# Kernel tuning notes

Hardware: AMD Instinct MI355X
Metric: run time of the kernel (lower is better)

Reference implementation:

```python
import jax, jax.numpy as jnp
import numpy as np

B, L = 1024, 1024
NCAT, NNUM = 20, 10
CAT_BUCKETS, SEQ_VOCAB = 100000, 50000
E, A, H, QH = 32, 128, 256, 256
TOPK = 30


def _init(key, shape, scale=0.02):
    return scale * jax.random.normal(key, shape, dtype=jnp.float32)


def setup_inputs() -> dict:
    key = jax.random.key(0)
    ks = jax.random.split(key, 24)
    z = lambda *s: jnp.zeros(s, dtype=jnp.float32)
    return {
        "cats": jax.random.randint(ks[0], (B, NCAT), 0, CAT_BUCKETS + 1),
        "nums": jax.random.normal(ks[1], (B, NNUM), dtype=jnp.float32),
        "seqs": jax.random.randint(ks[2], (B, L), 0, SEQ_VOCAB + 1),
        "tgt_ids": jax.random.randint(ks[3], (B,), 0, CAT_BUCKETS + 1),
        "cat_emb": _init(ks[4], (CAT_BUCKETS + 1, E)),
        "seq_emb": _init(ks[5], (SEQ_VOCAB + 1, E)),
        "Wnum": _init(ks[6], (NNUM, E)), "bnum": z(E),
        "Wq": _init(ks[7], (E, A)), "Wk": _init(ks[8], (E, A)), "Wv": _init(ks[9], (E, A)),
        "Wo": _init(ks[10], (A, E)), "bo": z(E),
        "Wpool": _init(ks[11], (NCAT * E, E)), "bpool": z(E),
        "Wmlp": _init(ks[12], (4 * E, H)), "bmlp": z(H),
        "q1_W1": _init(ks[13], (H, QH)), "q1_b1": z(QH),
        "q1_W2": _init(ks[14], (H, QH)), "q1_b2": z(QH),
        "q1_Wp": _init(ks[15], (QH, H)), "q1_bp": z(H),
        "q2_W1": _init(ks[16], (H, QH)), "q2_b1": z(QH),
        "q2_W2": _init(ks[17], (H, QH)), "q2_b2": z(QH),
        "q2_Wp": _init(ks[18], (QH, H)), "q2_bp": z(H),
        "Wout": _init(ks[19], (H, 1)), "bout": z(1),
    }


def _qnn(x, W1, b1, W2, b2, Wp, bp):
    # Quadratic neural block (QIN-style): Hadamard product of two linear maps,
    # projected back with a residual connection. Dropout is identity in eval.
    quad = (x @ W1 + b1) * (x @ W2 + b2)
    return x + quad @ Wp + bp


def reference(cats, nums, seqs, tgt_ids, cat_emb, seq_emb, Wnum, bnum, Wq, Wk, Wv,
              Wo, bo, Wpool, bpool, Wmlp, bmlp,
              q1_W1, q1_b1, q1_W2, q1_b2, q1_Wp, q1_bp,
              q2_W1, q2_b1, q2_W2, q2_b2, q2_Wp, q2_bp, Wout, bout):
    cat_e = cat_emb[cats]                                   # [B, NCAT, E]
    cat_pool = cat_e.reshape(cat_e.shape[0], -1) @ Wpool + bpool   # [B, E]
    num_e = nums @ Wnum + bnum                              # [B, E]
    tgt_e = cat_emb[tgt_ids]                                # [B, E] (tgt_emb shares cat_emb)
    seq_e = seq_emb[seqs]                                   # [B, L, E]

    q = tgt_e @ Wq                                          # [B, A]
    k = seq_e @ Wk                                          # [B, L, A]
    v = seq_e @ Wv                                          # [B, L, A]
    scores = jnp.einsum('ba,bla->bl', q, k) / jnp.sqrt(jnp.float32(A))

    # top-k + scatter mask + masked softmax == softmax over the top-k scores,
    # scattered implicitly via gather of the selected values.
    vals, idx = jax.lax.top_k(scores, TOPK)                 # [B, TOPK]
    w = jax.nn.softmax(vals, axis=1)                        # [B, TOPK]
    v_sel = jnp.take_along_axis(v, idx[:, :, None], axis=1)  # [B, TOPK, A]
    interest = jnp.einsum('bk,bka->ba', w, v_sel) @ Wo + bo  # [B, E]

    fused = jnp.concatenate([tgt_e, interest, cat_pool, num_e], axis=1)  # [B, 4E]
    h = jax.nn.relu(fused @ Wmlp + bmlp)                    # [B, H], dropout=eval
    h = _qnn(h, q1_W1, q1_b1, q1_W2, q1_b2, q1_Wp, q1_bp)
    h = _qnn(h, q2_W1, q2_b1, q2_W2, q2_b2, q2_Wp, q2_bp)
    return (h @ Wout + bout)[:, 0]                          # [B]
```

## Files before the change

### kernel.cpp

```cpp
#include <hip/hip_runtime.h>
#include <hip/hip_fp16.h>

#define B_ 1024
#define L_ 1024
#define NCAT_ 20
#define NNUM_ 10
#define E_ 32
#define A_ 128
#define H_ 256
#define TOPK_ 30
#define INV_SQRT_A 0.08838834764831845f

__device__ __forceinline__ void fma4(float4& a, float s, const float4 w) {
    a.x += s * w.x; a.y += s * w.y; a.z += s * w.z; a.w += s * w.w;
}
__device__ __forceinline__ float4 ldh4(const __half* p) {
    float2 rw = *(const float2*)p;
    const __half2* h = (const __half2*)&rw;
    float2 a = __half22float2(h[0]);
    float2 b = __half22float2(h[1]);
    return make_float4(a.x, a.y, b.x, b.y);
}
__device__ __forceinline__ void ldh24(const __half2* p, float4& w1, float4& w2) {
    float4 rw = *(const float4*)p;
    const __half2* h = (const __half2*)&rw;
    float2 f0 = __half22float2(h[0]), f1 = __half22float2(h[1]);
    float2 f2 = __half22float2(h[2]), f3 = __half22float2(h[3]);
    w1 = make_float4(f0.x, f1.x, f2.x, f3.x);
    w2 = make_float4(f0.y, f1.y, f2.y, f3.y);
}
__device__ __forceinline__ unsigned sortable(float f) {
    unsigned u = __float_as_uint(f);
    return (u & 0x80000000u) ? ~u : (u | 0x80000000u);
}
__device__ __forceinline__ float unsortable(unsigned s) {
    unsigned u = (s & 0x80000000u) ? (s ^ 0x80000000u) : ~s;
    return __uint_as_float(u);
}

#define K1_GRID 1356
__global__ __launch_bounds__(256) void fused_prep_kernel(
    const int* __restrict__ cats, const float* __restrict__ nums,
    const int* __restrict__ tgt_ids, const float* __restrict__ cat_emb,
    const float* __restrict__ Wnum, const float* __restrict__ bnum,
    const float* __restrict__ Wq, const float* __restrict__ Wk,
    const float* __restrict__ Wv, const float* __restrict__ Wo,
    const float* __restrict__ Wpool, const float* __restrict__ bpool,
    const float* __restrict__ seq_emb, const float* __restrict__ Wmlp,
    const float* __restrict__ q1W1, const float* __restrict__ q1W2,
    const float* __restrict__ q2W1, const float* __restrict__ q2W2,
    const float* __restrict__ q1Wp, const float* __restrict__ q2Wp,
    float* __restrict__ p_out, float* __restrict__ fused, float* __restrict__ M,
    __half2* __restrict__ seq_h2, __half2* __restrict__ Wmlp_h2,
    __half2* __restrict__ W12_1, __half2* __restrict__ W12_2,
    __half2* __restrict__ Wp1_h2, __half2* __restrict__ Wp2_h2)
{
    const int blk = blockIdx.x;
    const int t = threadIdx.x;

    if (blk < 256) {
        __shared__ float ce[4][NCAT_ * E_];
        __shared__ float tg[4][E_];
        __shared__ float nm[4][NNUM_];
        __shared__ float qs[4][A_];
        __shared__ float part[8][4][E_];
        const int r0 = blk * 4;

        for (int idx = t; idx < 640; idx += 256) {
            const int q = idx >> 3, f4 = idx & 7;
            const int row = q / 20, cat = q % 20;
            const int tok = cats[(r0 + row) * NCAT_ + cat];
            ((float4*)&ce[row][cat * 32])[f4] =
                ((const float4*)(cat_emb + (size_t)tok * 32))[f4];
        }
        if (t < 32) {
            const int row = t >> 3, f4 = t & 7;
            const int tok = tgt_ids[r0 + row];
            ((float4*)&tg[row][0])[f4] =
                ((const float4*)(cat_emb + (size_t)tok * 32))[f4];
        }
        if (t >= 64 && t < 104) {
            const int x = t - 64;
            nm[x / 10][x % 10] = nums[(r0 + x / 10) * NNUM_ + x % 10];
        }
        __syncthreads();

        {
            const int w = t >> 6, lane = t & 63;
            float q0 = 0.f, q1 = 0.f;
#pragma unroll
            for (int e = 0; e < E_; ++e) {
                float te = tg[w][e];
                q0 += te * Wq[e * A_ + lane];
                q1 += te * Wq[e * A_ + lane + 64];
            }
            qs[w][lane] = q0; qs[w][lane + 64] = q1;
        }

        {
            const int iseg = t >> 5;
            const int row = (t >> 3) & 3;
            const int c0 = (t & 7) * 4;
            float4 acc = make_float4(0.f, 0.f, 0.f, 0.f);
            const int i0 = iseg * 80;
            for (int i = i0; i < i0 + 80; ++i) {
                float4 wv = *(const float4*)(Wpool + i * 32 + c0);
                fma4(acc, ce[row][i], wv);
            }
            *(float4*)&part[iseg][row][c0] = acc;
        }
        __syncthreads();

        if (t < 128) {
            const int row = t >> 5, c = t & 31;
            const int b = r0 + row;
            float s = bpool[c];
#pragma unroll
            for (int g = 0; g < 8; ++g) s += part[g][row][c];
            fused[b * 128 + 64 + c] = s;
            fused[b * 128 + c] = tg[row][c];

            float ne = bnum[c];
#pragma unroll
            for (int n = 0; n < NNUM_; ++n) ne += nm[row][n] * Wnum[n * 32 + c];
            fused[b * 128 + 96 + c] = ne;

            float pv = 0.f;
#pragma unroll 8
            for (int a = 0; a < A_; ++a) pv += Wk[c * A_ + a] * qs[row][a];
            p_out[b * 32 + c] = pv;
        }
        return;
    }

    if (blk < 1280) {
        int x = (blk - 256) * 256 + t;
        for (; x < 800016; x += 1024 * 256) {
            float2 v = ((const float2*)seq_emb)[x];
            seq_h2[x] = __float22half2_rn(v);
        }
        return;
    }

    if (blk < 1284) {
        const int o = (blk - 1280) * 256 + t;
        const int j = o >> 5, e = o & 31;
        float sm = 0.f;
#pragma unroll 8
        for (int a = 0; a < A_; ++a) sm += Wv[j * A_ + a] * Wo[a * E_ + e];
        M[o] = sm;
        return;
    }

    if (blk < 1348) {
        int x = (blk - 1284) * 256 + t;
        for (; x < 65536; x += 64 * 256) {
            W12_1[x] = __float22half2_rn(make_float2(q1W1[x], q1W2[x]));
            W12_2[x] = __float22half2_rn(make_float2(q2W1[x], q2W2[x]));
        }
        return;
    }

    {
        int x = (blk - 1348) * 256 + t;
        for (; x < 16384; x += 8 * 256)
            Wmlp_h2[x] = __float22half2_rn(((const float2*)Wmlp)[x]);
        x = (blk - 1348) * 256 + t;
        for (; x < 32768; x += 8 * 256) {
            Wp1_h2[x] = __float22half2_rn(((const float2*)q1Wp)[x]);
            Wp2_h2[x] = __float22half2_rn(((const float2*)q2Wp)[x]);
        }
    }
}

#define RM 2
__global__ __launch_bounds__(512, 4) void score_mlp_kernel(
    const int* __restrict__ seqs, const __half* __restrict__ seq_h,
    const float* __restrict__ seq_emb, const float* __restrict__ p,
    const float* __restrict__ M, const float* __restrict__ bo,
    const float* __restrict__ fused,
    const __half* __restrict__ Wmlp_h, const float* __restrict__ bmlp,
    const __half2* __restrict__ W12_1, const float* __restrict__ b11,
    const float* __restrict__ b12, const __half* __restrict__ Wp1_h,
    const float* __restrict__ b1p,
    const __half2* __restrict__ W12_2, const float* __restrict__ b21,
    const float* __restrict__ b22, const __half* __restrict__ Wp2_h,
    const float* __restrict__ b2p,
    const float* __restrict__ Wout, const float* __restrict__ bout,
    float* __restrict__ out)
{
    const int b0 = blockIdx.x * RM;
    const int tid = threadIdx.x;

    __shared__ float sc[RM][L_];
    __shared__ float ps[RM][E_];
    __shared__ float sw[RM][32];
    __shared__ int   stok[RM][32];
    __shared__ float xs[RM][128];
    __shared__ float hs[RM][H_];
    __shared__ float ts[RM][H_];
    __shared__ float partA[8][RM][H_];
    __shared__ float partB[8][RM][H_];
    __shared__ float red[8];

    if (tid < RM * 32)
        ps[tid >> 5][tid & 31] = p[(b0 + (tid >> 5)) * 32 + (tid & 31)];
    __syncthreads();

    {
        const int row = tid >> 8;
        const int s = tid & 255;
        const int bb = b0 + row;
#pragma unroll
        for (int jj = 0; jj < 2; ++jj) {
            const int l1 = jj * 512 + s;
            const int l2 = l1 + 256;
            const int tok1 = seqs[bb * L_ + l1];
            const int tok2 = seqs[bb * L_ + l2];
            float4 buf[2][4];
            const float4* r1 = (const float4*)(seq_h + (size_t)tok1 * 32);
            const float4* r2 = (const float4*)(seq_h + (size_t)tok2 * 32);
#pragma unroll
            for (int i = 0; i < 4; ++i) buf[0][i] = r1[i];
#pragma unroll
            for (int i = 0; i < 4; ++i) buf[1][i] = r2[i];

            float acc0 = 0.f, acc1 = 0.f;
#pragma unroll
            for (int i = 0; i < 4; ++i) {
                const __half2* h1 = (const __half2*)&buf[0][i];
                const __half2* h2 = (const __half2*)&buf[1][i];
#pragma unroll
                for (int u = 0; u < 4; ++u) {
                    float2 f1 = __half22float2(h1[u]);
                    float2 f2 = __half22float2(h2[u]);
                    acc0 += f1.x * ps[row][i * 8 + 2 * u] + f1.y * ps[row][i * 8 + 2 * u + 1];
                    acc1 += f2.x * ps[row][i * 8 + 2 * u] + f2.y * ps[row][i * 8 + 2 * u + 1];
                }
            }
            sc[row][l1] = acc0 * INV_SQRT_A;
            sc[row][l2] = acc1 * INV_SQRT_A;
        }
    }
    if (tid < RM * 96) {
        const int r = tid / 96, c0 = tid % 96;
        const int c = (c0 < 32) ? c0 : (c0 + 32);
        xs[r][c] = fused[(b0 + r) * 128 + c];
    }
    __syncthreads();

    if (tid < RM * 64) {
        const int w = tid >> 6;
        const int lane = tid & 63;
        const int bb = b0 + w;

        unsigned long long key[16];
#pragma unroll
        for (int j = 0; j < 16; ++j) {
            const int l = j * 64 + lane;
            key[j] = ((unsigned long long)sortable(sc[w][l]) << 10)
                   | (unsigned)(1023 - l);
        }
#pragma unroll
        for (int a = 0; a < 15; ++a)
#pragma unroll
            for (int j = 0; j < 15 - a; ++j) {
                const bool swp = key[j] < key[j + 1];
                const unsigned long long hi = swp ? key[j + 1] : key[j];
                const unsigned long long lo = swp ? key[j] : key[j + 1];
                key[j] = hi; key[j + 1] = lo;
            }

        float myv = -1e30f; int myl = 0;
        unsigned long long front = key[0];
        for (int k = 0; k < TOPK_; ++k) {
            unsigned long long wk = front;
#pragma unroll
            for (int off = 32; off > 0; off >>= 1) {
                unsigned long long o = __shfl_xor(wk, off);
                if (o > wk) wk = o;
            }
            if (lane == k) {
                myv = unsortable((unsigned)(wk >> 10));
                myl = 1023 - (int)(wk & 1023);
            }
            if (front == wk) {
#pragma unroll
                for (int j = 0; j < 15; ++j) key[j] = key[j + 1];
                key[15] = 0ULL;
                front = key[0];
            }
        }

        float m = myv;
#pragma unroll
        for (int off = 32; off > 0; off >>= 1) m = fmaxf(m, __shfl_xor(m, off));
        float e = (lane < TOPK_) ? expf(myv - m) : 0.f;
        float s = e;
#pragma unroll
        for (int off = 32; off > 0; off >>= 1) s += __shfl_xor(s, off);
        if (lane < TOPK_) {
            sw[w][lane]   = e / s;
            stok[w][lane] = seqs[bb * L_ + myl];
        }

        if (lane < E_) {
            float acc = 0.f;
#pragma unroll
            for (int k = 0; k < TOPK_; ++k)
                acc += sw[w][k] * seq_emb[(size_t)stok[w][k] * 32 + lane];
            sc[w][lane] = acc;
        }
        if (lane < E_) {
            float acc = bo[lane];
#pragma unroll
            for (int j = 0; j < E_; ++j) acc += sc[w][j] * M[j * E_ + lane];
            xs[w][32 + lane] = acc;
        }
    }
    __syncthreads();

    const int cg = tid & 63;
    const int iseg = tid >> 6;
    const int c0 = cg * 4;
    const int rr = tid >> 8;
    const int rc = tid & 255;

    {
        float4 acc[RM];
#pragma unroll
        for (int r = 0; r < RM; ++r) acc[r] = make_float4(0.f, 0.f, 0.f, 0.f);
        const int i0 = iseg * 16;
#pragma unroll
        for (int iq = 0; iq < 4; ++iq) {
            const int i = i0 + iq * 4;
            float4 w[4], xv[RM];
#pragma unroll
            for (int u = 0; u < 4; ++u) w[u] = ldh4(Wmlp_h + (i + u) * H_ + c0);
#pragma unroll
            for (int r = 0; r < RM; ++r) xv[r] = *(const float4*)(&xs[r][i]);
#pragma unroll
            for (int r = 0; r < RM; ++r) {
                fma4(acc[r], xv[r].x, w[0]); fma4(acc[r], xv[r].y, w[1]);
                fma4(acc[r], xv[r].z, w[2]); fma4(acc[r], xv[r].w, w[3]);
            }
        }
#pragma unroll
        for (int r = 0; r < RM; ++r) *(float4*)&partA[iseg][r][c0] = acc[r];
    }
    __syncthreads();
    {
        float s = bmlp[rc];
#pragma unroll
        for (int sg = 0; sg < 8; ++sg) s += partA[sg][rr][rc];
        hs[rr][rc] = fmaxf(s, 0.f);
    }
    __syncthreads();

    const __half2* W12s[2] = { W12_1, W12_2 };
    const float* b1s[2] = { b11, b21 }; const float* b2s[2] = { b12, b22 };
    const __half* Wps[2] = { Wp1_h, Wp2_h }; const float* bps[2] = { b1p, b2p };

    for (int q = 0; q < 2; ++q) {
        const __half2* __restrict__ W12 = W12s[q];
        const __half*  __restrict__ Wp  = Wps[q];
        {
            float4 a1[RM], a2[RM];
#pragma unroll
            for (int r = 0; r < RM; ++r) {
                a1[r] = make_float4(0.f, 0.f, 0.f, 0.f);
                a2[r] = make_float4(0.f, 0.f, 0.f, 0.f);
            }
            const int i0 = iseg * 32;
#pragma unroll 2
            for (int iq = 0; iq < 8; ++iq) {
                const int i = i0 + iq * 4;
                float4 w1[4], w2[4], hv[RM];
#pragma unroll
                for (int u = 0; u < 4; ++u) ldh24(W12 + (i + u) * H_ + c0, w1[u], w2[u]);
#pragma unroll
                for (int r = 0; r < RM; ++r) hv[r] = *(const float4*)(&hs[r][i]);
#pragma unroll
                for (int r = 0; r < RM; ++r) {
                    fma4(a1[r], hv[r].x, w1[0]); fma4(a1[r], hv[r].y, w1[1]);
                    fma4(a1[r], hv[r].z, w1[2]); fma4(a1[r], hv[r].w, w1[3]);
                    fma4(a2[r], hv[r].x, w2[0]); fma4(a2[r], hv[r].y, w2[1]);
                    fma4(a2[r], hv[r].z, w2[2]); fma4(a2[r], hv[r].w, w2[3]);
                }
            }
#pragma unroll
            for (int r = 0; r < RM; ++r) {
                *(float4*)&partA[iseg][r][c0] = a1[r];
                *(float4*)&partB[iseg][r][c0] = a2[r];
            }
        }
        __syncthreads();
        {
            float t1 = b1s[q][rc], t2 = b2s[q][rc];
#pragma unroll
            for (int sg = 0; sg < 8; ++sg) {
                t1 += partA[sg][rr][rc];
                t2 += partB[sg][rr][rc];
            }
            ts[rr][rc] = t1 * t2;
        }
        __syncthreads();

        {
            float4 ap[RM];
#pragma unroll
            for (int r = 0; r < RM; ++r) ap[r] = make_float4(0.f, 0.f, 0.f, 0.f);
            const int i0 = iseg * 32;
#pragma unroll 2
            for (int iq = 0; iq < 8; ++iq) {
                const int i = i0 + iq * 4;
                float4 w[4], tv[RM];
#pragma unroll
                for (int u = 0; u < 4; ++u) w[u] = ldh4(Wp + (i + u) * H_ + c0);
#pragma unroll
                for (int r = 0; r < RM; ++r) tv[r] = *(const float4*)(&ts[r][i]);
#pragma unroll
                for (int r = 0; r < RM; ++r) {
                    fma4(ap[r], tv[r].x, w[0]); fma4(ap[r], tv[r].y, w[1]);
                    fma4(ap[r], tv[r].z, w[2]); fma4(ap[r], tv[r].w, w[3]);
                }
            }
#pragma unroll
            for (int r = 0; r < RM; ++r) *(float4*)&partA[iseg][r][c0] = ap[r];
        }
        __syncthreads();
        {
            float s = bps[q][rc];
#pragma unroll
            for (int sg = 0; sg < 8; ++sg) s += partA[sg][rr][rc];
            hs[rr][rc] += s;
        }
        __syncthreads();
    }

    {
        const int r = (tid >> 7) & (RM - 1);
        const int jj = tid & 127;
        float sum = 0.f;
        if (tid < RM * 128)
            sum = hs[r][jj] * Wout[jj] + hs[r][jj + 128] * Wout[jj + 128];
#pragma unroll
        for (int off = 32; off > 0; off >>= 1) sum += __shfl_down(sum, off);
        if (tid < RM * 128 && (tid & 63) == 0) red[tid >> 6] = sum;
        __syncthreads();
        if (tid < RM) out[b0 + tid] = red[2 * tid] + red[2 * tid + 1] + bout[0];
    }
}

extern "C" void kernel_launch(void* const* d_in, const int* in_sizes, int n_in,
                              void* d_out, int out_size, void* d_ws, size_t ws_size,
                              hipStream_t stream) {
    const int*   cats    = (const int*)d_in[0];
    const float* nums    = (const float*)d_in[1];
    const int*   seqs    = (const int*)d_in[2];
    const int*   tgt_ids = (const int*)d_in[3];
    const float* cat_emb = (const float*)d_in[4];
    const float* seq_emb = (const float*)d_in[5];
    const float* Wnum    = (const float*)d_in[6];
    const float* bnum    = (const float*)d_in[7];
    const float* Wq      = (const float*)d_in[8];
    const float* Wk      = (const float*)d_in[9];
    const float* Wv      = (const float*)d_in[10];
    const float* Wo      = (const float*)d_in[11];
    const float* bo      = (const float*)d_in[12];
    const float* Wpool   = (const float*)d_in[13];
    const float* bpool   = (const float*)d_in[14];
    const float* Wmlp    = (const float*)d_in[15];
    const float* bmlp    = (const float*)d_in[16];
    const float* q1_W1   = (const float*)d_in[17];
    const float* q1_b1   = (const float*)d_in[18];
    const float* q1_W2   = (const float*)d_in[19];
    const float* q1_b2   = (const float*)d_in[20];
    const float* q1_Wp   = (const float*)d_in[21];
    const float* q1_bp   = (const float*)d_in[22];
    const float* q2_W1   = (const float*)d_in[23];
    const float* q2_b1   = (const float*)d_in[24];
    const float* q2_W2   = (const float*)d_in[25];
    const float* q2_b2   = (const float*)d_in[26];
    const float* q2_Wp   = (const float*)d_in[27];
    const float* q2_bp   = (const float*)d_in[28];
    const float* Wout    = (const float*)d_in[29];
    const float* bout    = (const float*)d_in[30];

    float* ws = (float*)d_ws;
    float*   p       = ws;
    float*   fused   = ws + 32768;
    float*   M       = ws + 163840;
    __half2* seq_h2  = (__half2*)(ws + 164864);
    __half2* Wmlp_h2 = (__half2*)(ws + 964928);
    __half2* W12_1   = (__half2*)(ws + 981312);
    __half2* W12_2   = (__half2*)(ws + 1046848);
    __half2* Wp1_h2  = (__half2*)(ws + 1112384);
    __half2* Wp2_h2  = (__half2*)(ws + 1145152);

    float* out = (float*)d_out;

    fused_prep_kernel<<<K1_GRID, 256, 0, stream>>>(
        cats, nums, tgt_ids, cat_emb, Wnum, bnum, Wq, Wk, Wv, Wo,
        Wpool, bpool, seq_emb, Wmlp,
        q1_W1, q1_W2, q2_W1, q2_W2, q1_Wp, q2_Wp,
        p, fused, M, seq_h2, Wmlp_h2, W12_1, W12_2, Wp1_h2, Wp2_h2);

    score_mlp_kernel<<<B_ / RM, 512, 0, stream>>>(
        seqs, (const __half*)seq_h2, seq_emb, p, M, bo, fused,
        (const __half*)Wmlp_h2, bmlp,
        W12_1, q1_b1, q1_b2, (const __half*)Wp1_h2, q1_bp,
        W12_2, q2_b1, q2_b2, (const __half*)Wp2_h2, q2_bp,
        Wout, bout, out);
}
```

Before: 185.4 us.

## Split MLP into separate MFMA kernel with transposed fp16 weights

Moves the MLP and the two quadratic blocks out of the score/top-k kernel into a new kernel that processes 16 rows per block with 16x16x32 fp16 MFMA instructions. The prep kernel now writes transposed fp16 weight copies so MFMA B-operands can be loaded contiguously. The score kernel writes the interest vector to global memory instead of continuing with scalar FMA MLP work. This adds a kernel launch and a global round trip for the fused features, in exchange for much higher MLP throughput and less per-row weight re-reading.

```diff
diff --git a/kernel.cpp b/kernel.cpp
--- a/kernel.cpp
+++ b/kernel.cpp
@@ -11,24 +11,9 @@
 #define TOPK_ 30
 #define INV_SQRT_A 0.08838834764831845f
 
-__device__ __forceinline__ void fma4(float4& a, float s, const float4 w) {
-    a.x += s * w.x; a.y += s * w.y; a.z += s * w.z; a.w += s * w.w;
-}
-__device__ __forceinline__ float4 ldh4(const __half* p) {
-    float2 rw = *(const float2*)p;
-    const __half2* h = (const __half2*)&rw;
-    float2 a = __half22float2(h[0]);
-    float2 b = __half22float2(h[1]);
-    return make_float4(a.x, a.y, b.x, b.y);
-}
-__device__ __forceinline__ void ldh24(const __half2* p, float4& w1, float4& w2) {
-    float4 rw = *(const float4*)p;
-    const __half2* h = (const __half2*)&rw;
-    float2 f0 = __half22float2(h[0]), f1 = __half22float2(h[1]);
-    float2 f2 = __half22float2(h[2]), f3 = __half22float2(h[3]);
-    w1 = make_float4(f0.x, f1.x, f2.x, f3.x);
-    w2 = make_float4(f0.y, f1.y, f2.y, f3.y);
-}
+typedef _Float16 half8 __attribute__((ext_vector_type(8)));
+typedef float f32x4 __attribute__((ext_vector_type(4)));
+
 __device__ __forceinline__ unsigned sortable(float f) {
     unsigned u = __float_as_uint(f);
     return (u & 0x80000000u) ? ~u : (u | 0x80000000u);
@@ -36,6 +21,14 @@
 __device__ __forceinline__ float unsortable(unsigned s) {
     unsigned u = (s & 0x80000000u) ? (s ^ 0x80000000u) : ~s;
     return __uint_as_float(u);
+}
+__device__ __forceinline__ half8 cvt_h8(const float4 u, const float4 v) {
+    half8 a;
+    a[0] = (_Float16)u.x; a[1] = (_Float16)u.y;
+    a[2] = (_Float16)u.z; a[3] = (_Float16)u.w;
+    a[4] = (_Float16)v.x; a[5] = (_Float16)v.y;
+    a[6] = (_Float16)v.z; a[7] = (_Float16)v.w;
+    return a;
 }
 
 #define K1_GRID 1356
@@ -48,12 +41,14 @@
     const float* __restrict__ Wpool, const float* __restrict__ bpool,
     const float* __restrict__ seq_emb, const float* __restrict__ Wmlp,
     const float* __restrict__ q1W1, const float* __restrict__ q1W2,
+    const float* __restrict__ q1Wp,
     const float* __restrict__ q2W1, const float* __restrict__ q2W2,
-    const float* __restrict__ q1Wp, const float* __restrict__ q2Wp,
+    const float* __restrict__ q2Wp,
     float* __restrict__ p_out, float* __restrict__ fused, float* __restrict__ M,
-    __half2* __restrict__ seq_h2, __half2* __restrict__ Wmlp_h2,
-    __half2* __restrict__ W12_1, __half2* __restrict__ W12_2,
-    __half2* __restrict__ Wp1_h2, __half2* __restrict__ Wp2_h2)
+    __half2* __restrict__ seq_h2,
+    __half* __restrict__ WmlpT,
+    __half* __restrict__ W1T1, __half* __restrict__ W2T1, __half* __restrict__ WpT1,
+    __half* __restrict__ W1T2, __half* __restrict__ W2T2, __half* __restrict__ WpT2)
 {
     const int blk = blockIdx.x;
     const int t = threadIdx.x;
@@ -105,7 +100,8 @@
             const int i0 = iseg * 80;
             for (int i = i0; i < i0 + 80; ++i) {
                 float4 wv = *(const float4*)(Wpool + i * 32 + c0);
-                fma4(acc, ce[row][i], wv);
+                acc.x += ce[row][i] * wv.x; acc.y += ce[row][i] * wv.y;
+                acc.z += ce[row][i] * wv.z; acc.w += ce[row][i] * wv.w;
             }
             *(float4*)&part[iseg][row][c0] = acc;
         }
@@ -152,42 +148,47 @@
         return;
     }
 
-    if (blk < 1348) {
-        int x = (blk - 1284) * 256 + t;
-        for (; x < 65536; x += 64 * 256) {
-            W12_1[x] = __float22half2_rn(make_float2(q1W1[x], q1W2[x]));
-            W12_2[x] = __float22half2_rn(make_float2(q2W1[x], q2W2[x]));
-        }
-        return;
-    }
-
     {
-        int x = (blk - 1348) * 256 + t;
-        for (; x < 16384; x += 8 * 256)
-            Wmlp_h2[x] = __float22half2_rn(((const float2*)Wmlp)[x]);
-        x = (blk - 1348) * 256 + t;
-        for (; x < 32768; x += 8 * 256) {
-            Wp1_h2[x] = __float22half2_rn(((const float2*)q1Wp)[x]);
-            Wp2_h2[x] = __float22half2_rn(((const float2*)q2Wp)[x]);
+        int c = (blk - 1284) * 256 + t;
+        for (; c < 53248; c += 72 * 256) {
+            const float* src; __half* dst;
+            int n, k0, K;
+            if (c < 4096) {
+                n = c >> 4; k0 = (c & 15) << 3; K = 128;
+                src = Wmlp; dst = WmlpT;
+            } else {
+                const int c2 = c - 4096;
+                const int m = c2 >> 13, idx = c2 & 8191;
+                n = idx >> 5; k0 = (idx & 31) << 3; K = 256;
+                switch (m) {
+                    case 0: src = q1W1; dst = W1T1; break;
+                    case 1: src = q1W2; dst = W2T1; break;
+                    case 2: src = q1Wp; dst = WpT1; break;
+                    case 3: src = q2W1; dst = W1T2; break;
+                    case 4: src = q2W2; dst = W2T2; break;
+                    default: src = q2Wp; dst = WpT2; break;
+                }
+            }
+            float v[8];
+#pragma unroll
+            for (int i = 0; i < 8; ++i) v[i] = src[(size_t)(k0 + i) * 256 + n];
+            float4 wq;
+            __half2* hp = (__half2*)&wq;
+            hp[0] = __float22half2_rn(make_float2(v[0], v[1]));
+            hp[1] = __float22half2_rn(make_float2(v[2], v[3]));
+            hp[2] = __float22half2_rn(make_float2(v[4], v[5]));
+            hp[3] = __float22half2_rn(make_float2(v[6], v[7]));
+            *(float4*)(dst + (size_t)n * K + k0) = wq;
         }
     }
 }
 
 #define RM 2
-__global__ __launch_bounds__(512, 4) void score_mlp_kernel(
+__global__ __launch_bounds__(512) void score_topk_kernel(
     const int* __restrict__ seqs, const __half* __restrict__ seq_h,
     const float* __restrict__ seq_emb, const float* __restrict__ p,
     const float* __restrict__ M, const float* __restrict__ bo,
-    const float* __restrict__ fused,
-    const __half* __restrict__ Wmlp_h, const float* __restrict__ bmlp,
-    const __half2* __restrict__ W12_1, const float* __restrict__ b11,
-    const float* __restrict__ b12, const __half* __restrict__ Wp1_h,
-    const float* __restrict__ b1p,
-    const __half2* __restrict__ W12_2, const float* __restrict__ b21,
-    const float* __restrict__ b22, const __half* __restrict__ Wp2_h,
-    const float* __restrict__ b2p,
-    const float* __restrict__ Wout, const float* __restrict__ bout,
-    float* __restrict__ out)
+    float* __restrict__ fused)
 {
     const int b0 = blockIdx.x * RM;
     const int tid = threadIdx.x;
@@ -196,12 +197,6 @@
     __shared__ float ps[RM][E_];
     __shared__ float sw[RM][32];
     __shared__ int   stok[RM][32];
-    __shared__ float xs[RM][128];
-    __shared__ float hs[RM][H_];
-    __shared__ float ts[RM][H_];
-    __shared__ float partA[8][RM][H_];
-    __shared__ float partB[8][RM][H_];
-    __shared__ float red[8];
 
     if (tid < RM * 32)
         ps[tid >> 5][tid & 31] = p[(b0 + (tid >> 5)) * 32 + (tid & 31)];
@@ -242,11 +237,6 @@
             sc[row][l2] = acc1 * INV_SQRT_A;
         }
     }
-    if (tid < RM * 96) {
-        const int r = tid / 96, c0 = tid % 96;
-        const int c = (c0 < 32) ? c0 : (c0 + 32);
-        xs[r][c] = fused[(b0 + r) * 128 + c];
-    }
     __syncthreads();
 
     if (tid < RM * 64) {
@@ -315,140 +305,146 @@
             float acc = bo[lane];
 #pragma unroll
             for (int j = 0; j < E_; ++j) acc += sc[w][j] * M[j * E_ + lane];
-            xs[w][32 + lane] = acc;
+            fused[bb * 128 + 32 + lane] = acc;
+        }
+    }
+}
+
+#define GR 16
+#define HSP 260
+#define TSP 264
+__global__ __launch_bounds__(512) void mlp_mfma_kernel(
+    const float* __restrict__ fused,
+    const __half* __restrict__ WmlpT, const float* __restrict__ bmlp,
+    const __half* __restrict__ W1T1, const __half* __restrict__ W2T1,
+    const __half* __restrict__ WpT1,
+    const float* __restrict__ b11, const float* __restrict__ b12,
+    const float* __restrict__ b1p,
+    const __half* __restrict__ W1T2, const __half* __restrict__ W2T2,
+    const __half* __restrict__ WpT2,
+    const float* __restrict__ b21, const float* __restrict__ b22,
+    const float* __restrict__ b2p,
+    const float* __restrict__ Wout, const float* __restrict__ bout,
+    float* __restrict__ out)
+{
+    const int r0 = blockIdx.x * GR;
+    const int tid = threadIdx.x;
+    const int w = tid >> 6;
+    const int l = tid & 63;
+    const int lr = l & 15;
+    const int lk = l >> 4;
+    const int n0 = w * 32;
+
+    __shared__ float hs[GR][HSP];
+    __shared__ __half ts_h[GR][TSP];
+
+    f32x4 hC0, hC1;
+    const f32x4 zf = {0.f, 0.f, 0.f, 0.f};
+
+    {
+        half8 ax[4];
+        const float* xrow = fused + (size_t)(r0 + lr) * 128 + lk * 8;
+#pragma unroll
+        for (int ks = 0; ks < 4; ++ks) {
+            float4 u = *(const float4*)(xrow + ks * 32);
+            float4 v = *(const float4*)(xrow + ks * 32 + 4);
+            ax[ks] = cvt_h8(u, v);
+        }
+#pragma unroll
+        for (int t = 0; t < 2; ++t) {
+            f32x4 c = zf;
+            const __half* wb = WmlpT + (size_t)(n0 + 16 * t + lr) * 128 + lk * 8;
+#pragma unroll
+            for (int ks = 0; ks < 4; ++ks) {
+                half8 b = *(const half8*)(wb + ks * 32);
+                c = __builtin_amdgcn_mfma_f32_16x16x32_f16(ax[ks], b, c, 0, 0, 0);
+            }
+            const int j = n0 + 16 * t + lr;
+            const float bm = bmlp[j];
+#pragma unroll
+            for (int r = 0; r < 4; ++r) {
+                float vv = fmaxf(c[r] + bm, 0.f);
+                if (t == 0) hC0[r] = vv; else hC1[r] = vv;
+                hs[4 * lk + r][j] = vv;
+            }
         }
     }
     __syncthreads();
 
-    const int cg = tid & 63;
-    const int iseg = tid >> 6;
-    const int c0 = cg * 4;
-    const int rr = tid >> 8;
-    const int rc = tid & 255;
+#pragma unroll
+    for (int q = 0; q < 2; ++q) {
+        const __half* W1T = q ? W1T2 : W1T1;
+        const __half* W2T = q ? W2T2 : W2T1;
+        const __half* WpT = q ? WpT2 : WpT1;
+        const float* bb1 = q ? b21 : b11;
+        const float* bb2 = q ? b22 : b12;
+        const float* bbp = q ? b2p : b1p;
+
+        half8 ah[8];
+#pragma unroll
+        for (int ks = 0; ks < 8; ++ks) {
+            const float* hr = &hs[lr][ks * 32 + lk * 8];
+            float4 u = *(const float4*)hr;
+            float4 v = *(const float4*)(hr + 4);
+            ah[ks] = cvt_h8(u, v);
+        }
+#pragma unroll
+        for (int t = 0; t < 2; ++t) {
+            f32x4 t1 = zf, t2 = zf;
+            const __half* w1 = W1T + (size_t)(n0 + 16 * t + lr) * 256 + lk * 8;
+            const __half* w2 = W2T + (size_t)(n0 + 16 * t + lr) * 256 + lk * 8;
+#pragma unroll
+            for (int ks = 0; ks < 8; ++ks) {
+                half8 b1 = *(const half8*)(w1 + ks * 32);
+                t1 = __builtin_amdgcn_mfma_f32_16x16x32_f16(ah[ks], b1, t1, 0, 0, 0);
+                half8 b2 = *(const half8*)(w2 + ks * 32);
+                t2 = __builtin_amdgcn_mfma_f32_16x16x32_f16(ah[ks], b2, t2, 0, 0, 0);
+            }
+            const int j = n0 + 16 * t + lr;
+            const float v1 = bb1[j], v2 = bb2[j];
+#pragma unroll
+            for (int r = 0; r < 4; ++r) {
+                float tv = (t1[r] + v1) * (t2[r] + v2);
+                ts_h[4 * lk + r][j] = __float2half_rn(tv);
+            }
+        }
+        __syncthreads();
+
+        half8 pa[8];
+#pragma unroll
+        for (int ks = 0; ks < 8; ++ks)
+            pa[ks] = *(const half8*)&ts_h[lr][ks * 32 + lk * 8];
+#pragma unroll
+        for (int t = 0; t < 2; ++t) {
+            f32x4 c = (t == 0) ? hC0 : hC1;
+            const __half* wp = WpT + (size_t)(n0 + 16 * t + lr) * 256 + lk * 8;
+#pragma unroll
+            for (int ks = 0; ks < 8; ++ks) {
+                half8 b = *(const half8*)(wp + ks * 32);
+                c = __builtin_amdgcn_mfma_f32_16x16x32_f16(pa[ks], b, c, 0, 0, 0);
+            }
+            const int j = n0 + 16 * t + lr;
+            const float bp = bbp[j];
+#pragma unroll
+            for (int r = 0; r < 4; ++r) {
+                float vv = c[r] + bp;
+                if (t == 0) hC0[r] = vv; else hC1[r] = vv;
+                hs[4 * lk + r][j] = vv;
+            }
+        }
+        __syncthreads();
+    }
 
     {
-        float4 acc[RM];
-#pragma unroll
-        for (int r = 0; r < RM; ++r) acc[r] = make_float4(0.f, 0.f, 0.f, 0.f);
-        const int i0 = iseg * 16;
-#pragma unroll
-        for (int iq = 0; iq < 4; ++iq) {
-            const int i = i0 + iq * 4;
-            float4 w[4], xv[RM];
-#pragma unroll
-            for (int u = 0; u < 4; ++u) w[u] = ldh4(Wmlp_h + (i + u) * H_ + c0);
-#pragma unroll
-            for (int r = 0; r < RM; ++r) xv[r] = *(const float4*)(&xs[r][i]);
-#pragma unroll
-            for (int r = 0; r < RM; ++r) {
-                fma4(acc[r], xv[r].x, w[0]); fma4(acc[r], xv[r].y, w[1]);
-                fma4(acc[r], xv[r].z, w[2]); fma4(acc[r], xv[r].w, w[3]);
-            }
-        }
-#pragma unroll
-        for (int r = 0; r < RM; ++r) *(float4*)&partA[iseg][r][c0] = acc[r];
-    }
-    __syncthreads();
-    {
-        float s = bmlp[rc];
-#pragma unroll
-        for (int sg = 0; sg < 8; ++sg) s += partA[sg][rr][rc];
-        hs[rr][rc] = fmaxf(s, 0.f);
-    }
-    __syncthreads();
-
-    const __half2* W12s[2] = { W12_1, W12_2 };
-    const float* b1s[2] = { b11, b21 }; const float* b2s[2] = { b12, b22 };
-    const __half* Wps[2] = { Wp1_h, Wp2_h }; const float* bps[2] = { b1p, b2p };
-
-    for (int q = 0; q < 2; ++q) {
-        const __half2* __restrict__ W12 = W12s[q];
-        const __half*  __restrict__ Wp  = Wps[q];
-        {
-            float4 a1[RM], a2[RM];
-#pragma unroll
-            for (int r = 0; r < RM; ++r) {
-                a1[r] = make_float4(0.f, 0.f, 0.f, 0.f);
-                a2[r] = make_float4(0.f, 0.f, 0.f, 0.f);
-            }
-            const int i0 = iseg * 32;
-#pragma unroll 2
-            for (int iq = 0; iq < 8; ++iq) {
-                const int i = i0 + iq * 4;
-                float4 w1[4], w2[4], hv[RM];
-#pragma unroll
-                for (int u = 0; u < 4; ++u) ldh24(W12 + (i + u) * H_ + c0, w1[u], w2[u]);
-#pragma unroll
-                for (int r = 0; r < RM; ++r) hv[r] = *(const float4*)(&hs[r][i]);
-#pragma unroll
-                for (int r = 0; r < RM; ++r) {
-                    fma4(a1[r], hv[r].x, w1[0]); fma4(a1[r], hv[r].y, w1[1]);
-                    fma4(a1[r], hv[r].z, w1[2]); fma4(a1[r], hv[r].w, w1[3]);
-                    fma4(a2[r], hv[r].x, w2[0]); fma4(a2[r], hv[r].y, w2[1]);
-                    fma4(a2[r], hv[r].z, w2[2]); fma4(a2[r], hv[r].w, w2[3]);
-                }
-            }
-#pragma unroll
-            for (int r = 0; r < RM; ++r) {
-                *(float4*)&partA[iseg][r][c0] = a1[r];
-                *(float4*)&partB[iseg][r][c0] = a2[r];
-            }
-        }
-        __syncthreads();
-        {
-            float t1 = b1s[q][rc], t2 = b2s[q][rc];
-#pragma unroll
-            for (int sg = 0; sg < 8; ++sg) {
-                t1 += partA[sg][rr][rc];
-                t2 += partB[sg][rr][rc];
-            }
-            ts[rr][rc] = t1 * t2;
-        }
-        __syncthreads();
-
-        {
-            float4 ap[RM];
-#pragma unroll
-            for (int r = 0; r < RM; ++r) ap[r] = make_float4(0.f, 0.f, 0.f, 0.f);
-            const int i0 = iseg * 32;
-#pragma unroll 2
-            for (int iq = 0; iq < 8; ++iq) {
-                const int i = i0 + iq * 4;
-                float4 w[4], tv[RM];
-#pragma unroll
-                for (int u = 0; u < 4; ++u) w[u] = ldh4(Wp + (i + u) * H_ + c0);
-#pragma unroll
-                for (int r = 0; r < RM; ++r) tv[r] = *(const float4*)(&ts[r][i]);
-#pragma unroll
-                for (int r = 0; r < RM; ++r) {
-                    fma4(ap[r], tv[r].x, w[0]); fma4(ap[r], tv[r].y, w[1]);
-                    fma4(ap[r], tv[r].z, w[2]); fma4(ap[r], tv[r].w, w[3]);
-                }
-            }
-#pragma unroll
-            for (int r = 0; r < RM; ++r) *(float4*)&partA[iseg][r][c0] = ap[r];
-        }
-        __syncthreads();
-        {
-            float s = bps[q][rc];
-#pragma unroll
-            for (int sg = 0; sg < 8; ++sg) s += partA[sg][rr][rc];
-            hs[rr][rc] += s;
-        }
-        __syncthreads();
-    }
-
-    {
-        const int r = (tid >> 7) & (RM - 1);
-        const int jj = tid & 127;
-        float sum = 0.f;
-        if (tid < RM * 128)
-            sum = hs[r][jj] * Wout[jj] + hs[r][jj + 128] * Wout[jj + 128];
-#pragma unroll
-        for (int off = 32; off > 0; off >>= 1) sum += __shfl_down(sum, off);
-        if (tid < RM * 128 && (tid & 63) == 0) red[tid >> 6] = sum;
-        __syncthreads();
-        if (tid < RM) out[b0 + tid] = red[2 * tid] + red[2 * tid + 1] + bout[0];
+        const int i = tid >> 5;
+        const int seg = tid & 31;
+        const int cb = seg * 8;
+        float psum = 0.f;
+#pragma unroll
+        for (int u = 0; u < 8; ++u) psum += hs[i][cb + u] * Wout[cb + u];
+#pragma unroll
+        for (int off = 16; off > 0; off >>= 1) psum += __shfl_xor(psum, off);
+        if (seg == 0) out[r0 + i] = psum + bout[0];
     }
 }
 
@@ -492,24 +488,29 @@
     float*   fused   = ws + 32768;
     float*   M       = ws + 163840;
     __half2* seq_h2  = (__half2*)(ws + 164864);
-    __half2* Wmlp_h2 = (__half2*)(ws + 964928);
-    __half2* W12_1   = (__half2*)(ws + 981312);
-    __half2* W12_2   = (__half2*)(ws + 1046848);
-    __half2* Wp1_h2  = (__half2*)(ws + 1112384);
-    __half2* Wp2_h2  = (__half2*)(ws + 1145152);
+    __half*  WmlpT   = (__half*)(ws + 964928);
+    __half*  W1T1    = (__half*)(ws + 981312);
+    __half*  W2T1    = (__half*)(ws + 1014080);
+    __half*  WpT1    = (__half*)(ws + 1046848);
+    __half*  W1T2    = (__half*)(ws + 1079616);
+    __half*  W2T2    = (__half*)(ws + 1112384);
+    __half*  WpT2    = (__half*)(ws + 1145152);
 
     float* out = (float*)d_out;
 
     fused_prep_kernel<<<K1_GRID, 256, 0, stream>>>(
         cats, nums, tgt_ids, cat_emb, Wnum, bnum, Wq, Wk, Wv, Wo,
         Wpool, bpool, seq_emb, Wmlp,
-        q1_W1, q1_W2, q2_W1, q2_W2, q1_Wp, q2_Wp,
-        p, fused, M, seq_h2, Wmlp_h2, W12_1, W12_2, Wp1_h2, Wp2_h2);
-
-    score_mlp_kernel<<<B_ / RM, 512, 0, stream>>>(
-        seqs, (const __half*)seq_h2, seq_emb, p, M, bo, fused,
-        (const __half*)Wmlp_h2, bmlp,
-        W12_1, q1_b1, q1_b2, (const __half*)Wp1_h2, q1_bp,
-        W12_2, q2_b1, q2_b2, (const __half*)Wp2_h2, q2_bp,
+        q1_W1, q1_W2, q1_Wp, q2_W1, q2_W2, q2_Wp,
+        p, fused, M, seq_h2,
+        WmlpT, W1T1, W2T1, WpT1, W1T2, W2T2, WpT2);
+
+    score_topk_kernel<<<B_ / RM, 512, 0, stream>>>(
+        seqs, (const __half*)seq_h2, seq_emb, p, M, bo, fused);
+
+    mlp_mfma_kernel<<<B_ / GR, 512, 0, stream>>>(
+        fused, WmlpT, bmlp,
+        W1T1, W2T1, WpT1, q1_b1, q1_b2, q1_bp,
+        W1T2, W2T2, WpT2, q2_b1, q2_b2, q2_bp,
         Wout, bout, out);
 }
```

Result: slower. 200.6 us (+8.2%).

## Process four batch rows per 1024-thread block to amortize MLP weight loads

Applied to the files above, without the earlier changes.

Doubles rows per block from 2 to 4 and threads per block from 512 to 1024. Each half-precision MLP weight fetch is now reused across four rows, and the K dimension is split over 16 segments instead of 8. To fit shared memory, the two partial buffers are merged into one, so the quadratic block reduces its two branches one after the other with extra barriers. This gives fewer, larger blocks with lower occupancy flexibility, more synchronisation, and larger reductions per step.

```diff
diff --git a/kernel.cpp b/kernel.cpp
--- a/kernel.cpp
+++ b/kernel.cpp
@@ -173,8 +173,8 @@
     }
 }
 
-#define RM 2
-__global__ __launch_bounds__(512, 4) void score_mlp_kernel(
+#define RM 4
+__global__ __launch_bounds__(1024) void score_mlp_kernel(
     const int* __restrict__ seqs, const __half* __restrict__ seq_h,
     const float* __restrict__ seq_emb, const float* __restrict__ p,
     const float* __restrict__ M, const float* __restrict__ bo,
@@ -199,12 +199,10 @@
     __shared__ float xs[RM][128];
     __shared__ float hs[RM][H_];
     __shared__ float ts[RM][H_];
-    __shared__ float partA[8][RM][H_];
-    __shared__ float partB[8][RM][H_];
+    __shared__ float part[16][RM][H_];
     __shared__ float red[8];
 
-    if (tid < RM * 32)
-        ps[tid >> 5][tid & 31] = p[(b0 + (tid >> 5)) * 32 + (tid & 31)];
+    if (tid < 128) ps[tid >> 5][tid & 31] = p[(b0 + (tid >> 5)) * 32 + (tid & 31)];
     __syncthreads();
 
     {
@@ -242,14 +240,14 @@
             sc[row][l2] = acc1 * INV_SQRT_A;
         }
     }
-    if (tid < RM * 96) {
+    if (tid < 384) {
         const int r = tid / 96, c0 = tid % 96;
         const int c = (c0 < 32) ? c0 : (c0 + 32);
         xs[r][c] = fused[(b0 + r) * 128 + c];
     }
     __syncthreads();
 
-    if (tid < RM * 64) {
+    if (tid < 256) {
         const int w = tid >> 6;
         const int lane = tid & 63;
         const int bb = b0 + w;
@@ -330,9 +328,9 @@
         float4 acc[RM];
 #pragma unroll
         for (int r = 0; r < RM; ++r) acc[r] = make_float4(0.f, 0.f, 0.f, 0.f);
-        const int i0 = iseg * 16;
-#pragma unroll
-        for (int iq = 0; iq < 4; ++iq) {
+        const int i0 = iseg * 8;
+#pragma unroll
+        for (int iq = 0; iq < 2; ++iq) {
             const int i = i0 + iq * 4;
             float4 w[4], xv[RM];
 #pragma unroll
@@ -346,13 +344,13 @@
             }
         }
 #pragma unroll
-        for (int r = 0; r < RM; ++r) *(float4*)&partA[iseg][r][c0] = acc[r];
+        for (int r = 0; r < RM; ++r) *(float4*)&part[iseg][r][c0] = acc[r];
     }
     __syncthreads();
     {
         float s = bmlp[rc];
 #pragma unroll
-        for (int sg = 0; sg < 8; ++sg) s += partA[sg][rr][rc];
+        for (int sg = 0; sg < 16; ++sg) s += part[sg][rr][rc];
         hs[rr][rc] = fmaxf(s, 0.f);
     }
     __syncthreads();
@@ -364,16 +362,16 @@
     for (int q = 0; q < 2; ++q) {
         const __half2* __restrict__ W12 = W12s[q];
         const __half*  __restrict__ Wp  = Wps[q];
-        {
-            float4 a1[RM], a2[RM];
+        float4 a1[RM], a2[RM];
+        {
 #pragma unroll
             for (int r = 0; r < RM; ++r) {
                 a1[r] = make_float4(0.f, 0.f, 0.f, 0.f);
                 a2[r] = make_float4(0.f, 0.f, 0.f, 0.f);
             }
-            const int i0 = iseg * 32;
-#pragma unroll 2
-            for (int iq = 0; iq < 8; ++iq) {
+            const int i0 = iseg * 16;
+#pragma unroll
+            for (int iq = 0; iq < 4; ++iq) {
                 const int i = i0 + iq * 4;
                 float4 w1[4], w2[4], hv[RM];
 #pragma unroll
@@ -388,21 +386,25 @@
                     fma4(a2[r], hv[r].z, w2[2]); fma4(a2[r], hv[r].w, w2[3]);
                 }
             }
-#pragma unroll
-            for (int r = 0; r < RM; ++r) {
-                *(float4*)&partA[iseg][r][c0] = a1[r];
-                *(float4*)&partB[iseg][r][c0] = a2[r];
-            }
-        }
-        __syncthreads();
-        {
-            float t1 = b1s[q][rc], t2 = b2s[q][rc];
-#pragma unroll
-            for (int sg = 0; sg < 8; ++sg) {
-                t1 += partA[sg][rr][rc];
-                t2 += partB[sg][rr][rc];
-            }
-            ts[rr][rc] = t1 * t2;
+        }
+#pragma unroll
+        for (int r = 0; r < RM; ++r) *(float4*)&part[iseg][r][c0] = a1[r];
+        __syncthreads();
+        {
+            float t1 = b1s[q][rc];
+#pragma unroll
+            for (int sg = 0; sg < 16; ++sg) t1 += part[sg][rr][rc];
+            ts[rr][rc] = t1;
+        }
+        __syncthreads();
+#pragma unroll
+        for (int r = 0; r < RM; ++r) *(float4*)&part[iseg][r][c0] = a2[r];
+        __syncthreads();
+        {
+            float t2 = b2s[q][rc];
+#pragma unroll
+            for (int sg = 0; sg < 16; ++sg) t2 += part[sg][rr][rc];
+            ts[rr][rc] = ts[rr][rc] * t2;
         }
         __syncthreads();
 
@@ -410,9 +412,9 @@
             float4 ap[RM];
 #pragma unroll
             for (int r = 0; r < RM; ++r) ap[r] = make_float4(0.f, 0.f, 0.f, 0.f);
-            const int i0 = iseg * 32;
-#pragma unroll 2
-            for (int iq = 0; iq < 8; ++iq) {
+            const int i0 = iseg * 16;
+#pragma unroll
+            for (int iq = 0; iq < 4; ++iq) {
                 const int i = i0 + iq * 4;
                 float4 w[4], tv[RM];
 #pragma unroll
@@ -426,27 +428,26 @@
                 }
             }
 #pragma unroll
-            for (int r = 0; r < RM; ++r) *(float4*)&partA[iseg][r][c0] = ap[r];
+            for (int r = 0; r < RM; ++r) *(float4*)&part[iseg][r][c0] = ap[r];
         }
         __syncthreads();
         {
             float s = bps[q][rc];
 #pragma unroll
-            for (int sg = 0; sg < 8; ++sg) s += partA[sg][rr][rc];
+            for (int sg = 0; sg < 16; ++sg) s += part[sg][rr][rc];
             hs[rr][rc] += s;
         }
         __syncthreads();
     }
 
     {
-        const int r = (tid >> 7) & (RM - 1);
-        const int jj = tid & 127;
-        float sum = 0.f;
-        if (tid < RM * 128)
-            sum = hs[r][jj] * Wout[jj] + hs[r][jj + 128] * Wout[jj + 128];
-#pragma unroll
-        for (int off = 32; off > 0; off >>= 1) sum += __shfl_down(sum, off);
-        if (tid < RM * 128 && (tid & 63) == 0) red[tid >> 6] = sum;
+        if (tid < 512) {
+            const int r = tid >> 7, jj = tid & 127;
+            float sum = hs[r][jj] * Wout[jj] + hs[r][jj + 128] * Wout[jj + 128];
+#pragma unroll
+            for (int off = 32; off > 0; off >>= 1) sum += __shfl_down(sum, off);
+            if ((tid & 63) == 0) red[tid >> 6] = sum;
+        }
         __syncthreads();
         if (tid < RM) out[b0 + tid] = red[2 * tid] + red[2 * tid + 1] + bout[0];
     }
@@ -506,7 +507,7 @@
         q1_W1, q1_W2, q2_W1, q2_W2, q1_Wp, q2_Wp,
         p, fused, M, seq_h2, Wmlp_h2, W12_1, W12_2, Wp1_h2, Wp2_h2);
 
-    score_mlp_kernel<<<B_ / RM, 512, 0, stream>>>(
+    score_mlp_kernel<<<B_ / RM, 1024, 0, stream>>>(
         seqs, (const __half*)seq_h2, seq_emb, p, M, bo, fused,
         (const __half*)Wmlp_h2, bmlp,
         W12_1, q1_b1, q1_b2, (const __half*)Wp1_h2, q1_bp,
```

Result: slower. 211.0 us (+13.8%).
